# Optimization experiments

Hardware: AMD Instinct MI355X
Metric: run time of the kernel (lower is better)

Reference implementation:

```python
import jax, jax.numpy as jnp
import numpy as np

B, S, D, H = 4, 1024, 1024, 16
HD = D // H  # per-head dim = 64
NEG = -10000000000.0


def setup_inputs() -> dict:
    key = jax.random.key(0)
    ks = jax.random.split(key, 12)
    q = jax.random.normal(ks[0], (B, S, D), jnp.float32)
    k = jax.random.normal(ks[1], (B, S, D), jnp.float32)
    v = jax.random.normal(ks[2], (B, S, D), jnp.float32)
    mask = jax.random.randint(ks[3], (B, S, S), 0, 2).astype(jnp.int32)
    sc = 1.0 / np.sqrt(D)
    Wq = jax.random.normal(ks[4], (H, D, HD), jnp.float32) * sc
    bq = jnp.zeros((H, HD), jnp.float32)
    Wk = jax.random.normal(ks[5], (H, D, HD), jnp.float32) * sc
    bk = jnp.zeros((H, HD), jnp.float32)
    Wv = jax.random.normal(ks[6], (H, D, HD), jnp.float32) * sc
    bv = jnp.zeros((H, HD), jnp.float32)
    Wo = jax.random.normal(ks[7], (D, D), jnp.float32) * sc
    bo = jnp.zeros((D,), jnp.float32)
    return {"query": q, "key": k, "value": v, "attention_mask": mask,
            "Wq": Wq, "bq": bq, "Wk": Wk, "bk": bk, "Wv": Wv, "bv": bv,
            "Wo": Wo, "bo": bo}


def reference(query, key, value, attention_mask, Wq, bq, Wk, bk, Wv, bv, Wo, bo):
    # batched per-head projections: [B,S,D] x [H,D,E] -> [B,H,S,E]
    q = jnp.einsum('bsd,hde->bhse', query, Wq) + bq[None, :, None, :]
    k = jnp.einsum('bsd,hde->bhse', key, Wk) + bk[None, :, None, :]
    v = jnp.einsum('bsd,hde->bhse', value, Wv) + bv[None, :, None, :]
    # NOTE: scale uses key_dim (model_size = full D), faithful to source
    score = jnp.einsum('bhse,bhte->bhst', q, k) / jnp.sqrt(jnp.float32(D))
    m = attention_mask.astype(jnp.float32)[:, None, :, :]  # [B,1,S,S]
    score = score + (1.0 - m) * NEG
    attn = jax.nn.softmax(score, axis=-1) * m  # double masking
    heads = jnp.einsum('bhst,bhte->bhse', attn, v)  # [B,H,S,E]
    # concat heads along feature dim (head order preserved)
    heads = heads.transpose(0, 2, 1, 3).reshape(B, S, D)
    return heads @ Wo + bo
```

## Files before the change

kernel.cpp:

```cpp
#include <hip/hip_runtime.h>

#define B_ 4
#define S_ 1024
#define D_ 1024
#define H_ 16
#define E_ 64
#define BS_ (B_*S_)
#define BHSE_ (B_*H_*S_*E_)

typedef __attribute__((ext_vector_type(8))) short bf16x8;
typedef __attribute__((ext_vector_type(4))) float f32x4;
typedef __attribute__((ext_vector_type(4))) unsigned int u32x4;

__device__ __forceinline__ unsigned short f2bf(float f) {
    unsigned int x = __float_as_uint(f);
    x = (x + 0x7FFFu + ((x >> 16) & 1u)) >> 16;
    return (unsigned short)x;
}
__device__ __forceinline__ float bf2f(unsigned short u) {
    return __uint_as_float(((unsigned int)u) << 16);
}
__device__ __forceinline__ float ldin(const void* p, size_t i, int isb) {
    return isb ? bf2f(((const unsigned short*)p)[i]) : ((const float*)p)[i];
}

__device__ __forceinline__ unsigned int cvtpk(float lo, float hi) {
    unsigned int r;
    asm("v_cvt_pk_bf16_f32 %0, %1, %2" : "=v"(r) : "v"(lo), "v"(hi));
    return r;
}
__device__ __forceinline__ unsigned int bperm(int srclane4, unsigned int v) {
    return (unsigned int)__builtin_amdgcn_ds_bpermute(srclane4, (int)v);
}
__device__ __forceinline__ bf16x8 u4bf(u32x4 w) {
    union { u32x4 u; bf16x8 h; } c; c.u = w; return c.h;
}

#if __has_builtin(__builtin_amdgcn_exp2f)
#define EXP2(x) __builtin_amdgcn_exp2f(x)
#else
#define EXP2(x) __expf((x) * 0.6931471805599453f)
#endif

__device__ __forceinline__ void gl2lds16(const void* g, void* l) {
    __builtin_amdgcn_global_load_lds(
        (const __attribute__((address_space(1))) void*)g,
        (__attribute__((address_space(3))) void*)l, 16, 0, 0);
}

__device__ __forceinline__ int detect_isb(const unsigned int* q) {
    unsigned int wv = q[threadIdx.x & 63];
    unsigned int lo = wv & 0xFFFFu;
    unsigned int e = (lo >> 7) & 0xFFu;
    int ok = (lo == 0u) || (e >= 100u && e <= 145u);
    return __popcll(__ballot(ok)) >= 48;
}

__global__ __launch_bounds__(256) void preproc(
        const void* q_, const void* k_, const void* v_, const int* mask,
        const void* Wq, const void* Wk, const void* Wv, const void* Wo,
        const void* bq_, const void* bk_, const void* bv_, const void* bo_,
        unsigned short* WT, float* biases, unsigned long long* packT,
        unsigned short* Aconv) {
    __shared__ unsigned short Tt[64][72];
    const int isb = detect_isb((const unsigned int*)q_);
    const int blk = blockIdx.x, t = threadIdx.x;

    if (blk < 1024) {
        const int c0 = blk & 15, r0 = ((blk >> 4) & 15) * 64, z = blk >> 8;
        const void* src = (z == 0) ? Wq : (z == 1) ? Wk : (z == 2) ? Wv : Wo;
        {
            int dl = t >> 2, qc = t & 3;
            size_t base;
            if (z < 3) base = (size_t)c0 * 65536 + (size_t)(r0 + dl) * 64 + qc * 16;
            else       base = (size_t)(r0 + dl) * 1024 + (size_t)c0 * 64 + qc * 16;
            if (isb) {
                const unsigned short* s = (const unsigned short*)src + base;
                bf16x8 a0 = *(const bf16x8*)s, a1 = *(const bf16x8*)(s + 8);
#pragma unroll
                for (int j = 0; j < 8; j++) {
                    Tt[qc * 16 + j][dl] = (unsigned short)a0[j];
                    Tt[qc * 16 + 8 + j][dl] = (unsigned short)a1[j];
                }
            } else {
                const float* s = (const float*)src + base;
#pragma unroll
                for (int j = 0; j < 16; j++) Tt[qc * 16 + j][dl] = f2bf(s[j]);
            }
        }
        __syncthreads();
        {
            int el = t >> 2, qc = t & 3;
            size_t dst = (size_t)z * D_ * D_ + (size_t)(c0 * 64 + el) * D_ + r0 + qc * 16;
            *(bf16x8*)&WT[dst]     = *(const bf16x8*)&Tt[el][qc * 16];
            *(bf16x8*)&WT[dst + 8] = *(const bf16x8*)&Tt[el][qc * 16 + 8];
        }
        if (z == 3 && ((blk >> 4) & 15) == 0 && c0 < 4) {
            const void* bs = (c0 == 0) ? bq_ : (c0 == 1) ? bk_
                           : (c0 == 2) ? bv_ : bo_;
#pragma unroll
            for (int j = 0; j < 4; j++) {
                int i = t * 4 + j;
                biases[c0 * 1024 + i] = ldin(bs, i, isb);
            }
        }
    } else if (blk < 5120) {
        int unit = (blk - 1024) * 4 + (t >> 6);
        int lane = t & 63;
        int b = unit >> 12, rem = unit & 4095, s0 = (rem >> 4) * 4, kt = rem & 15;
        const int* mb = mask + ((size_t)b * 1024 + s0) * 1024 + kt * 64 + lane;
        unsigned long long bits[4];
#pragma unroll
        for (int j = 0; j < 4; j++) bits[j] = __ballot(mb[j * 1024] != 0);
        if (lane < 4) {
            unsigned long long bb = (lane == 0) ? bits[0] : (lane == 1) ? bits[1]
                                  : (lane == 2) ? bits[2] : bits[3];
            packT[((size_t)b * 16 + kt) * 1024 + s0 + lane] = bb;
        }
    } else {
        if (isb) return;
        int blk2 = blk - 5120;
        const int z = blk2 >> 11;
        const float* s = (z == 0) ? (const float*)q_ : (z == 1) ? (const float*)k_
                                                                : (const float*)v_;
        const size_t i = ((size_t)(blk2 & 2047) * 256 + t) * 8;
        f32x4 a0 = *(const f32x4*)(s + i);
        f32x4 a1 = *(const f32x4*)(s + i + 4);
        bf16x8 o;
#pragma unroll
        for (int j = 0; j < 4; j++) {
            o[j]     = (short)f2bf(a0[j]);
            o[4 + j] = (short)f2bf(a1[j]);
        }
        *(bf16x8*)&Aconv[(size_t)z * ((size_t)BS_ * D_) + i] = o;
    }
}

template<int BM, int BN, int MODE, int MINW>
__global__ __launch_bounds__(256, MINW) void gemm_k(
        const void* A0, const void* A1, const void* A2, const unsigned short* Aconv,
        const unsigned short* BtB, const float* biasB, void* dstB,
        const unsigned int* qdet) {
    constexpr int TOT16 = (BM + BN) * 32;
    constexpr int CALLS = TOT16 / 512;
    constexpr int CPW = CALLS / 4;
    constexpr int MT = BM / 32;
    constexpr int NT = BN / 32;
    __shared__ unsigned short buf[2][TOT16];

    const int fl = detect_isb(qdet);
    const int t = threadIdx.x, lane = t & 63, w = t >> 6;
    const int lm = lane & 15, q4 = lane >> 4;
    const int wm = w >> 1, wn = w & 1;
    const int lr = lane >> 2;
    const int ls = lane & 3;
    const int lg = ls ^ ((lr >> 1) & 3);

    const unsigned short* Abf;
    const unsigned short* Bt;
    const float* bias;
    int z = 0, m0, n0, phase;
    if (MODE == 0) {
        int bid = blockIdx.x + gridDim.x * (blockIdx.y + gridDim.y * blockIdx.z);
        int xcd = bid & 7, idx = bid >> 3;
        z = idx >> 5;
        int r = idx & 31;
        int mt = (xcd << 2) + (r & 3);
        int nt = r >> 2;
        m0 = mt * BM; n0 = nt * BN;
        phase = (nt * 13 + z * 5) & 31;
        const void* Ain = (z == 0) ? A0 : (z == 1 ? A1 : A2);
        Abf = fl ? (const unsigned short*)Ain
                 : Aconv + (size_t)z * ((size_t)BS_ * D_);
        Bt = BtB + (size_t)z * D_ * D_;
        bias = biasB + z * 1024;
    } else {
        Abf = (const unsigned short*)A0;
        Bt = BtB; bias = biasB;
        int bid = blockIdx.x + (blockIdx.y << 5);
        int xcd = bid & 7, idx = bid >> 3;
        m0 = ((xcd << 2) + (idx & 3)) * BM;
        n0 = (idx >> 2) * BN;
        phase = ((idx >> 2) * 13) & 31;
    }

    auto stage = [&](int kk, int bi) {
#pragma unroll
        for (int i = 0; i < CPW; ++i) {
            int c = w * CPW + i;
            int row = c * 16 + lr;
            const unsigned short* g;
            if (row < BM)
                g = Abf + (size_t)(m0 + row) * D_ + kk + lg * 8;
            else
                g = Bt + (size_t)(n0 + row - BM) * D_ + kk + lg * 8;
            gl2lds16(g, &buf[bi][c * 512]);
        }
    };

    f32x4 acc[MT][NT];
#pragma unroll
    for (int i = 0; i < MT; i++)
#pragma unroll
        for (int j = 0; j < NT; j++) acc[i][j] = (f32x4){0.f, 0.f, 0.f, 0.f};

    stage((phase & 31) * 32, 0);
    for (int it = 0; it < D_ / 32; ++it) {
        const int bi = it & 1;
        __syncthreads();
        if (it < D_ / 32 - 1) stage(((it + 1 + phase) & 31) * 32, bi ^ 1);

        const unsigned short* As = buf[bi];
        const unsigned short* Bs = buf[bi] + BM * 32;
        bf16x8 af[MT], bv[NT];
#pragma unroll
        for (int mt = 0; mt < MT; mt++) {
            int row = wm * (BM / 2) + mt * 16 + lm;
            af[mt] = *(const bf16x8*)&As[row * 32 + (q4 ^ ((row >> 1) & 3)) * 8];
        }
#pragma unroll
        for (int nt = 0; nt < NT; nt++) {
            int row = wn * (BN / 2) + nt * 16 + lm;
            bv[nt] = *(const bf16x8*)&Bs[row * 32 + (q4 ^ ((row >> 1) & 3)) * 8];
        }
#pragma unroll
        for (int mt = 0; mt < MT; mt++)
#pragma unroll
            for (int nt = 0; nt < NT; nt++)
                acc[mt][nt] = __builtin_amdgcn_mfma_f32_16x16x32_bf16(
                    af[mt], bv[nt], acc[mt][nt], 0, 0, 0);
    }

#pragma unroll
    for (int mt = 0; mt < MT; mt++)
#pragma unroll
        for (int nt = 0; nt < NT; nt++) {
            int N = n0 + wn * (BN / 2) + nt * 16 + lm;
            int Mb = m0 + wm * (BM / 2) + mt * 16 + q4 * 4;
            if (MODE == 0 && z == 2) {
                int bb = Mb >> 10, sb = Mb & 1023, hh = N >> 6, e = N & 63;
                unsigned long long hv = 0;
#pragma unroll
                for (int r = 0; r < 4; r++)
                    hv |= (unsigned long long)f2bf(acc[mt][nt][r] + bias[N]) << (16 * r);
                unsigned short* d16 = (unsigned short*)dstB + (size_t)2 * BHSE_;
                *(unsigned long long*)&d16[(((size_t)(bb * H_ + hh) * E_ + e) << 10) + sb] = hv;
            } else {
#pragma unroll
                for (int r = 0; r < 4; r++) {
                    int M = Mb + r;
                    float v = acc[mt][nt][r] + bias[N];
                    if (MODE == 0) {
                        int bb = M >> 10, s = M & 1023, hh = N >> 6, e = N & 63;
                        unsigned short* d16 = (unsigned short*)dstB + (size_t)z * BHSE_;
                        d16[((size_t)(bb * H_ + hh) * S_ + s) * E_ + e] = f2bf(v);
                    } else {
                        size_t idx = (size_t)M * D_ + N;
                        if (fl) ((unsigned short*)dstB)[idx] = f2bf(v);
                        else    ((float*)dstB)[idx] = v;
                    }
                }
            }
        }
}

__global__ __launch_bounds__(512, 4) void attn64(
        const unsigned short* Qp, const unsigned short* Kp, const unsigned short* VpT,
        const unsigned long long* packT, unsigned short* heads) {
    __shared__ unsigned short KT[3][4096];
    __shared__ unsigned short VT[3][4096];

    const int bid = blockIdx.x + (blockIdx.y << 3) + (blockIdx.z << 7);
    const int xcd = bid & 7, idx = bid >> 3;
    const int qt = idx >> 3;
    const int hb = xcd * 8 + (idx & 7);
    const int h = hb & 15, b = hb >> 4;

    const int t = threadIdx.x, w = t >> 6, lane = t & 63, lm = lane & 15, q4 = lane >> 4;
    const size_t bh = ((size_t)b * H_ + h) * S_ * E_;
    const unsigned short* Qb = Qp + bh;
    const unsigned short* Kb = Kp + bh;
    const unsigned short* Vb = VpT + bh;
    const int q0 = qt * 128 + w * 16;

    const int l3 = lane >> 3, l7 = lane & 7;
    const int kLaneOff = l3 * 64 + (l7 ^ l3) * 8;
    const int vLaneOff = l3 * 1024 + (l7 ^ l3) * 8;

    const int sw = lm & 7;
    const int c0 = (q4 ^ sw) * 8, c1 = ((q4 ^ 4) ^ sw) * 8;

    const int srcA4 = ((lane & 15) | ((lane & 16) << 1)) << 2;
    const int srcB4 = srcA4 + 64;
    const bool selHi = (lane & 32) != 0;

    bf16x8 bq0 = *(const bf16x8*)&Qb[(size_t)(q0 + lm) * E_ + q4 * 8];
    bf16x8 bq1 = *(const bf16x8*)&Qb[(size_t)(q0 + lm) * E_ + 32 + q4 * 8];

    bf16x8 ones;
#pragma unroll
    for (int j = 0; j < 8; j++) ones[j] = (short)0x3F80;

    f32x4 oacc[4];
#pragma unroll
    for (int i = 0; i < 4; i++) oacc[i] = (f32x4){0.f, 0.f, 0.f, 0.f};
    f32x4 accL = (f32x4){0.f, 0.f, 0.f, 0.f};
    float mrun = -3.0e38f;
    const float scale2 = 0.03125f * 1.4426950408889634f;

#define STAGE(ktile, kdst, vdst)                                              \
    {                                                                         \
        int k0s = (ktile) * 64;                                               \
        _Pragma("unroll")                                                     \
        for (int i_ = 0; i_ < 2; ++i_) {                                      \
            int c_ = w * 2 + i_;                                              \
            if (c_ < 8) {                                                     \
                gl2lds16(Kb + (size_t)k0s * 64 + c_ * 512 + kLaneOff,         \
                         (kdst) + c_ * 512);                                  \
            } else {                                                          \
                int cc_ = c_ - 8;                                             \
                gl2lds16(Vb + (size_t)cc_ * 8192 + k0s + vLaneOff,            \
                         (vdst) + cc_ * 512);                                 \
            }                                                                 \
        }                                                                     \
    }

    auto QK = [&](const unsigned short* kb, f32x4* st) {
#pragma unroll
        for (int jt = 0; jt < 4; ++jt) {
            const unsigned short* kr = &kb[(jt * 16 + lm) * 64];
            bf16x8 ka0 = *(const bf16x8*)&kr[c0];
            bf16x8 ka1 = *(const bf16x8*)&kr[c1];
            f32x4 zz = (f32x4){0.f, 0.f, 0.f, 0.f};
            zz = __builtin_amdgcn_mfma_f32_16x16x32_bf16(ka0, bq0, zz, 0, 0, 0);
            zz = __builtin_amdgcn_mfma_f32_16x16x32_bf16(ka1, bq1, zz, 0, 0, 0);
            st[jt] = zz;
        }
    };

    unsigned short *kA = &KT[0][0], *kB = &KT[1][0], *kC = &KT[2][0];
    unsigned short *vA = &VT[0][0], *vB = &VT[1][0], *vC = &VT[2][0];

    STAGE(0, kA, vA)
    STAGE(1, kB, vB)
    unsigned long long mk = packT[(size_t)b * 16 * 1024 + q0 + lm];
    __syncthreads();
    f32x4 stC[4], stN[4];
    QK(kA, stC);

    for (int kt = 0; kt < S_ / 64; ++kt) {
        __syncthreads();
        unsigned long long mknext = 0;
        if (kt < 15) mknext = packT[((size_t)b * 16 + kt + 1) * 1024 + q0 + lm];
        if (kt < 14) STAGE(kt + 2, kC, vC)
        if (kt < 15) QK(kB, stN);

        float mx0 = fmaxf(fmaxf(stC[0][0], stC[0][1]), fmaxf(stC[0][2], stC[0][3]));
        float mx1 = fmaxf(fmaxf(stC[1][0], stC[1][1]), fmaxf(stC[1][2], stC[1][3]));
        float mx2 = fmaxf(fmaxf(stC[2][0], stC[2][1]), fmaxf(stC[2][2], stC[2][3]));
        float mx3 = fmaxf(fmaxf(stC[3][0], stC[3][1]), fmaxf(stC[3][2], stC[3][3]));
        float tmx = fmaxf(fmaxf(mx0, mx1), fmaxf(mx2, mx3));
        tmx = fmaxf(tmx, __shfl_xor(tmx, 16, 64));
        tmx = fmaxf(tmx, __shfl_xor(tmx, 32, 64));
        float pmax = tmx * scale2;

        if (!__all(pmax - mrun <= 8.f)) {
            float mnew = fmaxf(mrun, pmax);
            float alpha = EXP2(mrun - mnew);
            accL = accL * alpha;
#pragma unroll
            for (int nt = 0; nt < 4; nt++) oacc[nt] = oacc[nt] * alpha;
            mrun = mnew;
        }
        const float mneg = -mrun;

        unsigned int mn = (unsigned int)(mk >> (q4 * 4));
        unsigned int mh = (unsigned int)(mk >> (q4 * 4 + 32));

        unsigned int cl[8];
#pragma unroll
        for (int jt = 0; jt < 4; ++jt) {
            unsigned int mm = (jt & 2) ? mh : mn;
            const int sh = (jt & 1) * 16;
            float p0 = EXP2(fmaf(stC[jt][0], scale2, mneg));
            float p1 = EXP2(fmaf(stC[jt][1], scale2, mneg));
            float p2 = EXP2(fmaf(stC[jt][2], scale2, mneg));
            float p3 = EXP2(fmaf(stC[jt][3], scale2, mneg));
            p0 = (mm & (1u << (sh + 0))) ? p0 : 0.f;
            p1 = (mm & (1u << (sh + 1))) ? p1 : 0.f;
            p2 = (mm & (1u << (sh + 2))) ? p2 : 0.f;
            p3 = (mm & (1u << (sh + 3))) ? p3 : 0.f;
            cl[jt * 2]     = cvtpk(p0, p1);
            cl[jt * 2 + 1] = cvtpk(p2, p3);
        }

        u32x4 w0, w1;
        {
            unsigned int aA0 = bperm(srcA4, cl[0]), aA2 = bperm(srcA4, cl[2]);
            unsigned int aA1 = bperm(srcA4, cl[1]), aA3 = bperm(srcA4, cl[3]);
            unsigned int aB0 = bperm(srcB4, cl[0]), aB2 = bperm(srcB4, cl[2]);
            unsigned int aB1 = bperm(srcB4, cl[1]), aB3 = bperm(srcB4, cl[3]);
            w0 = (u32x4){selHi ? aA2 : aA0, selHi ? aA3 : aA1,
                         selHi ? aB2 : aB0, selHi ? aB3 : aB1};
            unsigned int bA0 = bperm(srcA4, cl[4]), bA2 = bperm(srcA4, cl[6]);
            unsigned int bA1 = bperm(srcA4, cl[5]), bA3 = bperm(srcA4, cl[7]);
            unsigned int bB0 = bperm(srcB4, cl[4]), bB2 = bperm(srcB4, cl[6]);
            unsigned int bB1 = bperm(srcB4, cl[5]), bB3 = bperm(srcB4, cl[7]);
            w1 = (u32x4){selHi ? bA2 : bA0, selHi ? bA3 : bA1,
                         selHi ? bB2 : bB0, selHi ? bB3 : bB1};
        }
        bf16x8 bp0 = u4bf(w0);
        bf16x8 bp1 = u4bf(w1);

        accL = __builtin_amdgcn_mfma_f32_16x16x32_bf16(ones, bp0, accL, 0, 0, 0);
        accL = __builtin_amdgcn_mfma_f32_16x16x32_bf16(ones, bp1, accL, 0, 0, 0);

#pragma unroll
        for (int nt = 0; nt < 4; nt++) {
            const unsigned short* vr = &vA[(nt * 16 + lm) * 64];
            bf16x8 va0 = *(const bf16x8*)&vr[c0];
            bf16x8 va1 = *(const bf16x8*)&vr[c1];
            oacc[nt] = __builtin_amdgcn_mfma_f32_16x16x32_bf16(va0, bp0, oacc[nt], 0, 0, 0);
            oacc[nt] = __builtin_amdgcn_mfma_f32_16x16x32_bf16(va1, bp1, oacc[nt], 0, 0, 0);
        }

        unsigned short* tp;
        tp = kA; kA = kB; kB = kC; kC = tp;
        tp = vA; vA = vB; vB = vC; vC = tp;
        if (kt < 15) {
            stC[0] = stN[0]; stC[1] = stN[1]; stC[2] = stN[2]; stC[3] = stN[3];
        }
        mk = mknext;
    }

    float inv = 1.0f / accL[0];
#pragma unroll
    for (int nt = 0; nt < 4; nt++) {
        unsigned int lo = cvtpk(oacc[nt][0] * inv, oacc[nt][1] * inv);
        unsigned int hi = cvtpk(oacc[nt][2] * inv, oacc[nt][3] * inv);
        unsigned long long hv = (unsigned long long)lo | ((unsigned long long)hi << 32);
        *(unsigned long long*)&heads[(size_t)(b * S_ + q0 + lm) * D_ + h * E_ + nt * 16 + q4 * 4] = hv;
    }
}

extern "C" void kernel_launch(void* const* d_in, const int* in_sizes, int n_in,
                              void* d_out, int out_size, void* d_ws, size_t ws_size,
                              hipStream_t stream) {
    char* ws = (char*)d_ws;
    unsigned short* WT = (unsigned short*)(ws + 256);
    unsigned short* WqT = WT;
    unsigned short* WoT = WT + (size_t)3 * D_ * D_;
    float* biases = (float*)(WT + (size_t)4 * D_ * D_);
    float* bq = biases;
    float* bo = biases + 3 * 1024;
    unsigned short* Qp = (unsigned short*)(biases + 4 * 1024);
    unsigned short* Kp = Qp + (size_t)BHSE_;
    unsigned short* Vp = Kp + (size_t)BHSE_;
    unsigned short* heads = Vp + (size_t)BHSE_;
    unsigned long long* packT = (unsigned long long*)(heads + (size_t)BHSE_);
    unsigned short* Aconv = (unsigned short*)(packT + (size_t)B_ * 16 * S_);

    preproc<<<11264, 256, 0, stream>>>(
        d_in[0], d_in[1], d_in[2], (const int*)d_in[3],
        d_in[4], d_in[6], d_in[8], d_in[10],
        d_in[5], d_in[7], d_in[9], d_in[11],
        WT, biases, packT, Aconv);
    gemm_k<128, 128, 0, 3><<<dim3(32, 8, 3), 256, 0, stream>>>(
        d_in[0], d_in[1], d_in[2], Aconv, WqT, bq, Qp,
        (const unsigned int*)d_in[0]);
    attn64<<<dim3(8, 16, 4), 512, 0, stream>>>(Qp, Kp, Vp, packT, heads);
    gemm_k<128, 64, 1, 4><<<dim3(32, 16, 1), 256, 0, stream>>>(
        heads, nullptr, nullptr, nullptr, WoT, bo, d_out,
        (const unsigned int*)d_in[0]);
}
```

Baseline: 226.0 us.

## Process 128-key tiles with double-buffered LDS instead of 64-key triple buffering

Restructures the attention inner loop to handle 128 keys per iteration using two LDS buffers of twice the size, in place of 64-key tiles with a three-deep ring that pipelined QK for the next tile. This halves the number of iterations, barriers and online-softmax max/rescale checks per query block. In exchange it drops the software-pipelined QK overlap, raises register pressure from holding two sub-tiles of scores, and keeps total LDS similar (64KB vs 48KB), which may reduce occupancy.

```diff
diff --git a/kernel.cpp b/kernel.cpp
--- a/kernel.cpp
+++ b/kernel.cpp
@@ -267,8 +267,8 @@
 __global__ __launch_bounds__(512, 4) void attn64(
         const unsigned short* Qp, const unsigned short* Kp, const unsigned short* VpT,
         const unsigned long long* packT, unsigned short* heads) {
-    __shared__ unsigned short KT[3][4096];
-    __shared__ unsigned short VT[3][4096];
+    __shared__ unsigned short KT[2][8192];
+    __shared__ unsigned short VT[2][8192];
 
     const int bid = blockIdx.x + (blockIdx.y << 3) + (blockIdx.z << 7);
     const int xcd = bid & 7, idx = bid >> 3;
@@ -308,58 +308,60 @@
     float mrun = -3.0e38f;
     const float scale2 = 0.03125f * 1.4426950408889634f;
 
-#define STAGE(ktile, kdst, vdst)                                              \
+#define STAGE(tile, bufi)                                                     \
     {                                                                         \
-        int k0s = (ktile) * 64;                                               \
+        int k0s = (tile) * 128;                                               \
         _Pragma("unroll")                                                     \
-        for (int i_ = 0; i_ < 2; ++i_) {                                      \
-            int c_ = w * 2 + i_;                                              \
-            if (c_ < 8) {                                                     \
+        for (int i_ = 0; i_ < 4; ++i_) {                                      \
+            int c_ = w * 4 + i_;                                              \
+            if (c_ < 16) {                                                    \
                 gl2lds16(Kb + (size_t)k0s * 64 + c_ * 512 + kLaneOff,         \
-                         (kdst) + c_ * 512);                                  \
+                         &KT[bufi][c_ * 512]);                                \
             } else {                                                          \
-                int cc_ = c_ - 8;                                             \
-                gl2lds16(Vb + (size_t)cc_ * 8192 + k0s + vLaneOff,            \
-                         (vdst) + cc_ * 512);                                 \
+                int cc_ = c_ - 16, sub_ = cc_ >> 3, ec_ = cc_ & 7;            \
+                gl2lds16(Vb + (size_t)ec_ * 8192 + k0s + sub_ * 64 + vLaneOff,\
+                         &VT[bufi][sub_ * 4096 + ec_ * 512]);                 \
             }                                                                 \
         }                                                                     \
     }
 
-    auto QK = [&](const unsigned short* kb, f32x4* st) {
-#pragma unroll
-        for (int jt = 0; jt < 4; ++jt) {
-            const unsigned short* kr = &kb[(jt * 16 + lm) * 64];
-            bf16x8 ka0 = *(const bf16x8*)&kr[c0];
-            bf16x8 ka1 = *(const bf16x8*)&kr[c1];
-            f32x4 zz = (f32x4){0.f, 0.f, 0.f, 0.f};
-            zz = __builtin_amdgcn_mfma_f32_16x16x32_bf16(ka0, bq0, zz, 0, 0, 0);
-            zz = __builtin_amdgcn_mfma_f32_16x16x32_bf16(ka1, bq1, zz, 0, 0, 0);
-            st[jt] = zz;
-        }
-    };
-
-    unsigned short *kA = &KT[0][0], *kB = &KT[1][0], *kC = &KT[2][0];
-    unsigned short *vA = &VT[0][0], *vB = &VT[1][0], *vC = &VT[2][0];
-
-    STAGE(0, kA, vA)
-    STAGE(1, kB, vB)
-    unsigned long long mk = packT[(size_t)b * 16 * 1024 + q0 + lm];
-    __syncthreads();
-    f32x4 stC[4], stN[4];
-    QK(kA, stC);
-
-    for (int kt = 0; kt < S_ / 64; ++kt) {
+    STAGE(0, 0)
+    unsigned long long mk0 = packT[(size_t)b * 16 * 1024 + q0 + lm];
+    unsigned long long mk1 = packT[((size_t)b * 16 + 1) * 1024 + q0 + lm];
+
+    for (int T = 0; T < S_ / 128; ++T) {
+        const int bufi = T & 1;
         __syncthreads();
-        unsigned long long mknext = 0;
-        if (kt < 15) mknext = packT[((size_t)b * 16 + kt + 1) * 1024 + q0 + lm];
-        if (kt < 14) STAGE(kt + 2, kC, vC)
-        if (kt < 15) QK(kB, stN);
-
-        float mx0 = fmaxf(fmaxf(stC[0][0], stC[0][1]), fmaxf(stC[0][2], stC[0][3]));
-        float mx1 = fmaxf(fmaxf(stC[1][0], stC[1][1]), fmaxf(stC[1][2], stC[1][3]));
-        float mx2 = fmaxf(fmaxf(stC[2][0], stC[2][1]), fmaxf(stC[2][2], stC[2][3]));
-        float mx3 = fmaxf(fmaxf(stC[3][0], stC[3][1]), fmaxf(stC[3][2], stC[3][3]));
-        float tmx = fmaxf(fmaxf(mx0, mx1), fmaxf(mx2, mx3));
+        unsigned long long mkn0 = 0, mkn1 = 0;
+        if (T < 7) {
+            STAGE(T + 1, bufi ^ 1)
+            mkn0 = packT[((size_t)b * 16 + 2 * T + 2) * 1024 + q0 + lm];
+            mkn1 = packT[((size_t)b * 16 + 2 * T + 3) * 1024 + q0 + lm];
+        }
+
+        f32x4 st[2][4];
+#pragma unroll
+        for (int sub = 0; sub < 2; ++sub)
+#pragma unroll
+            for (int jt = 0; jt < 4; ++jt) {
+                const unsigned short* kr = &KT[bufi][(sub * 64 + jt * 16 + lm) * 64];
+                bf16x8 ka0 = *(const bf16x8*)&kr[c0];
+                bf16x8 ka1 = *(const bf16x8*)&kr[c1];
+                f32x4 zz = (f32x4){0.f, 0.f, 0.f, 0.f};
+                zz = __builtin_amdgcn_mfma_f32_16x16x32_bf16(ka0, bq0, zz, 0, 0, 0);
+                zz = __builtin_amdgcn_mfma_f32_16x16x32_bf16(ka1, bq1, zz, 0, 0, 0);
+                st[sub][jt] = zz;
+            }
+
+        float tmx = -3.0e38f;
+#pragma unroll
+        for (int sub = 0; sub < 2; ++sub)
+#pragma unroll
+            for (int jt = 0; jt < 4; ++jt) {
+                float a = fmaxf(st[sub][jt][0], st[sub][jt][1]);
+                float c = fmaxf(st[sub][jt][2], st[sub][jt][3]);
+                tmx = fmaxf(tmx, fmaxf(a, c));
+            }
         tmx = fmaxf(tmx, __shfl_xor(tmx, 16, 64));
         tmx = fmaxf(tmx, __shfl_xor(tmx, 32, 64));
         float pmax = tmx * scale2;
@@ -374,63 +376,65 @@
         }
         const float mneg = -mrun;
 
-        unsigned int mn = (unsigned int)(mk >> (q4 * 4));
-        unsigned int mh = (unsigned int)(mk >> (q4 * 4 + 32));
-
-        unsigned int cl[8];
-#pragma unroll
-        for (int jt = 0; jt < 4; ++jt) {
-            unsigned int mm = (jt & 2) ? mh : mn;
-            const int sh = (jt & 1) * 16;
-            float p0 = EXP2(fmaf(stC[jt][0], scale2, mneg));
-            float p1 = EXP2(fmaf(stC[jt][1], scale2, mneg));
-            float p2 = EXP2(fmaf(stC[jt][2], scale2, mneg));
-            float p3 = EXP2(fmaf(stC[jt][3], scale2, mneg));
-            p0 = (mm & (1u << (sh + 0))) ? p0 : 0.f;
-            p1 = (mm & (1u << (sh + 1))) ? p1 : 0.f;
-            p2 = (mm & (1u << (sh + 2))) ? p2 : 0.f;
-            p3 = (mm & (1u << (sh + 3))) ? p3 : 0.f;
-            cl[jt * 2]     = cvtpk(p0, p1);
-            cl[jt * 2 + 1] = cvtpk(p2, p3);
-        }
-
-        u32x4 w0, w1;
-        {
-            unsigned int aA0 = bperm(srcA4, cl[0]), aA2 = bperm(srcA4, cl[2]);
-            unsigned int aA1 = bperm(srcA4, cl[1]), aA3 = bperm(srcA4, cl[3]);
-            unsigned int aB0 = bperm(srcB4, cl[0]), aB2 = bperm(srcB4, cl[2]);
-            unsigned int aB1 = bperm(srcB4, cl[1]), aB3 = bperm(srcB4, cl[3]);
-            w0 = (u32x4){selHi ? aA2 : aA0, selHi ? aA3 : aA1,
-                         selHi ? aB2 : aB0, selHi ? aB3 : aB1};
-            unsigned int bA0 = bperm(srcA4, cl[4]), bA2 = bperm(srcA4, cl[6]);
-            unsigned int bA1 = bperm(srcA4, cl[5]), bA3 = bperm(srcA4, cl[7]);
-            unsigned int bB0 = bperm(srcB4, cl[4]), bB2 = bperm(srcB4, cl[6]);
-            unsigned int bB1 = bperm(srcB4, cl[5]), bB3 = bperm(srcB4, cl[7]);
-            w1 = (u32x4){selHi ? bA2 : bA0, selHi ? bA3 : bA1,
-                         selHi ? bB2 : bB0, selHi ? bB3 : bB1};
-        }
-        bf16x8 bp0 = u4bf(w0);
-        bf16x8 bp1 = u4bf(w1);
-
-        accL = __builtin_amdgcn_mfma_f32_16x16x32_bf16(ones, bp0, accL, 0, 0, 0);
-        accL = __builtin_amdgcn_mfma_f32_16x16x32_bf16(ones, bp1, accL, 0, 0, 0);
-
-#pragma unroll
-        for (int nt = 0; nt < 4; nt++) {
-            const unsigned short* vr = &vA[(nt * 16 + lm) * 64];
-            bf16x8 va0 = *(const bf16x8*)&vr[c0];
-            bf16x8 va1 = *(const bf16x8*)&vr[c1];
-            oacc[nt] = __builtin_amdgcn_mfma_f32_16x16x32_bf16(va0, bp0, oacc[nt], 0, 0, 0);
-            oacc[nt] = __builtin_amdgcn_mfma_f32_16x16x32_bf16(va1, bp1, oacc[nt], 0, 0, 0);
-        }
-
-        unsigned short* tp;
-        tp = kA; kA = kB; kB = kC; kC = tp;
-        tp = vA; vA = vB; vB = vC; vC = tp;
-        if (kt < 15) {
-            stC[0] = stN[0]; stC[1] = stN[1]; stC[2] = stN[2]; stC[3] = stN[3];
-        }
-        mk = mknext;
+        unsigned int cl[2][8];
+#pragma unroll
+        for (int sub = 0; sub < 2; ++sub) {
+            unsigned long long mk = sub ? mk1 : mk0;
+            unsigned int mn = (unsigned int)(mk >> (q4 * 4));
+            unsigned int mh = (unsigned int)(mk >> (q4 * 4 + 32));
+#pragma unroll
+            for (int jt = 0; jt < 4; ++jt) {
+                unsigned int mm = (jt & 2) ? mh : mn;
+                const int sh = (jt & 1) * 16;
+                float p0 = EXP2(fmaf(st[sub][jt][0], scale2, mneg));
+                float p1 = EXP2(fmaf(st[sub][jt][1], scale2, mneg));
+                float p2 = EXP2(fmaf(st[sub][jt][2], scale2, mneg));
+                float p3 = EXP2(fmaf(st[sub][jt][3], scale2, mneg));
+                p0 = (mm & (1u << (sh + 0))) ? p0 : 0.f;
+                p1 = (mm & (1u << (sh + 1))) ? p1 : 0.f;
+                p2 = (mm & (1u << (sh + 2))) ? p2 : 0.f;
+                p3 = (mm & (1u << (sh + 3))) ? p3 : 0.f;
+                cl[sub][jt * 2]     = cvtpk(p0, p1);
+                cl[sub][jt * 2 + 1] = cvtpk(p2, p3);
+            }
+        }
+
+#pragma unroll
+        for (int sub = 0; sub < 2; ++sub) {
+            unsigned int* c = cl[sub];
+            u32x4 w0, w1;
+            {
+                unsigned int aA0 = bperm(srcA4, c[0]), aA2 = bperm(srcA4, c[2]);
+                unsigned int aA1 = bperm(srcA4, c[1]), aA3 = bperm(srcA4, c[3]);
+                unsigned int aB0 = bperm(srcB4, c[0]), aB2 = bperm(srcB4, c[2]);
+                unsigned int aB1 = bperm(srcB4, c[1]), aB3 = bperm(srcB4, c[3]);
+                w0 = (u32x4){selHi ? aA2 : aA0, selHi ? aA3 : aA1,
+                             selHi ? aB2 : aB0, selHi ? aB3 : aB1};
+                unsigned int bA0 = bperm(srcA4, c[4]), bA2 = bperm(srcA4, c[6]);
+                unsigned int bA1 = bperm(srcA4, c[5]), bA3 = bperm(srcA4, c[7]);
+                unsigned int bB0 = bperm(srcB4, c[4]), bB2 = bperm(srcB4, c[6]);
+                unsigned int bB1 = bperm(srcB4, c[5]), bB3 = bperm(srcB4, c[7]);
+                w1 = (u32x4){selHi ? bA2 : bA0, selHi ? bA3 : bA1,
+                             selHi ? bB2 : bB0, selHi ? bB3 : bB1};
+            }
+            bf16x8 bp0 = u4bf(w0);
+            bf16x8 bp1 = u4bf(w1);
+
+            accL = __builtin_amdgcn_mfma_f32_16x16x32_bf16(ones, bp0, accL, 0, 0, 0);
+            accL = __builtin_amdgcn_mfma_f32_16x16x32_bf16(ones, bp1, accL, 0, 0, 0);
+
+            const unsigned short* vbase = &VT[bufi][sub * 4096];
+#pragma unroll
+            for (int nt = 0; nt < 4; nt++) {
+                const unsigned short* vr = &vbase[(nt * 16 + lm) * 64];
+                bf16x8 va0 = *(const bf16x8*)&vr[c0];
+                bf16x8 va1 = *(const bf16x8*)&vr[c1];
+                oacc[nt] = __builtin_amdgcn_mfma_f32_16x16x32_bf16(va0, bp0, oacc[nt], 0, 0, 0);
+                oacc[nt] = __builtin_amdgcn_mfma_f32_16x16x32_bf16(va1, bp1, oacc[nt], 0, 0, 0);
+            }
+        }
+
+        mk0 = mkn0; mk1 = mkn1;
     }
 
     float inv = 1.0f / accL[0];
```

New measurement: 224.3 us. About the same (-0.7%).
